# Kernel optimization log

Measured on AMD Instinct MI355X. Metric: run time of the kernel, lower is better.

## Reference

```python
import jax, jax.numpy as jnp
import numpy as np


def setup_inputs() -> dict:
    key = jax.random.key(0)
    k1, k2, k3, k4 = jax.random.split(key, 4)
    B, C, H, W = 8, 256, 64, 64
    x = jax.random.normal(k1, (B, C, H, W), dtype=jnp.float32)
    wq = jax.random.normal(k2, (1, C), dtype=jnp.float32) * (1.0 / np.sqrt(C))
    wk = jax.random.normal(k3, (1, C), dtype=jnp.float32) * (1.0 / np.sqrt(C))
    wv = jax.random.normal(k4, (C, C), dtype=jnp.float32) * (1.0 / np.sqrt(C))
    gamma = jnp.zeros((1,), dtype=jnp.float32)
    return {"x": x, "wq": wq, "wk": wk, "wv": wv, "gamma": gamma}


def reference(x, wq, wk, wv, gamma):
    B, C, H, W = x.shape
    N = H * W
    xf = x.reshape(B, C, N)                      # [B, C, N]
    # 1x1 convs == channel matmuls
    f = jnp.einsum('oc,bcn->bon', wq, xf)        # [B, 1, N]
    g = jnp.einsum('oc,bcn->bon', wk, xf)        # [B, 1, N]
    h = jnp.einsum('oc,bcn->bon', wv, xf)        # [B, C, N]
    # scores[b, i, j] = f[b, 0, i] * g[b, 0, j]  -> [B, N, N]
    scores = jnp.einsum('bi,bj->bij', f[:, 0, :], g[:, 0, :])
    # softmax over dim=1 (rows), matching torch F.softmax(..., dim=1)
    beta = jax.nn.softmax(scores, axis=1)        # [B, N, N]
    gam = gamma[0]
    o = (1.0 - gam) * jnp.einsum('bcn,bnm->bcm', h, beta) + gam * xf
    return o.reshape(B, C, H, W)
```

## Files before the change

### kernel.cpp

```cpp
#include <hip/hip_runtime.h>
#include <math.h>

#define BQ 8
#define CQ 256
#define NQ 4096
#define MT 128
#define NSUP 64

typedef short s16x8 __attribute__((ext_vector_type(8)));
typedef short s16x4 __attribute__((ext_vector_type(4)));
typedef float f32x4 __attribute__((ext_vector_type(4)));
typedef unsigned int uint;

static __device__ __forceinline__ float4 ld4(const float* p) { return *(const float4*)p; }

static constexpr float LOG2E = 1.4426950408889634f;

static __device__ __forceinline__ short f2bf(float f) {
    return __builtin_bit_cast(short, (__bf16)f);
}
static __device__ __forceinline__ uint fkey(float f) {
    uint b = __builtin_bit_cast(uint, f);
    return b ^ (0x80000000u | (uint)((int)b >> 31));
}
static __device__ __forceinline__ float fdec(uint u) {
    uint b = (u & 0x80000000u) ? (u ^ 0x80000000u) : ~u;
    return __builtin_bit_cast(float, b);
}

__global__ void k_fg(const float* __restrict__ x, const float* __restrict__ wq,
                     const float* __restrict__ wk, float* __restrict__ fs,
                     float* __restrict__ g, short* __restrict__ xbf,
                     uint* __restrict__ fmxu, uint* __restrict__ fmnu) {
    int b = blockIdx.y;
    int t = threadIdx.x;
    int nl = (t & 31) * 2;
    int cg = t >> 5;
    int n = blockIdx.x * 64 + nl;
    const float* xb = x + (size_t)b * CQ * NQ + n;
    uint* xo = (uint*)(xbf + (size_t)b * CQ * NQ + n);
    float f0 = 0.f, f1 = 0.f, g0 = 0.f, g1 = 0.f;
    int c0 = cg * 32;
#pragma unroll 8
    for (int c = c0; c < c0 + 32; ++c) {
        float2 v = *(const float2*)&xb[(size_t)c * NQ];
        f0 = fmaf(wq[c], v.x, f0);
        f1 = fmaf(wq[c], v.y, f1);
        g0 = fmaf(wk[c], v.x, g0);
        g1 = fmaf(wk[c], v.y, g1);
        uint p = (uint)(unsigned short)f2bf(v.x) | ((uint)(unsigned short)f2bf(v.y) << 16);
        xo[c * (NQ / 2)] = p;
    }
    __shared__ float sf[8][64], sg2[8][64];
    sf[cg][nl] = f0;  sf[cg][nl + 1] = f1;
    sg2[cg][nl] = g0; sg2[cg][nl + 1] = g1;
    __syncthreads();
    if (t < 64) {
        float f = 0.f, gg = 0.f;
#pragma unroll
        for (int i = 0; i < 8; ++i) { f += sf[i][t]; gg += sg2[i][t]; }
        f *= LOG2E;
        fs[b * NQ + blockIdx.x * 64 + t] = f;
        g[b * NQ + blockIdx.x * 64 + t]  = gg;
        float mx = f, mn = f;
#pragma unroll
        for (int off = 32; off; off >>= 1) {
            mx = fmaxf(mx, __shfl_xor(mx, off));
            mn = fminf(mn, __shfl_xor(mn, off));
        }
        if (t == 0) {
            atomicMax(&fmxu[b], fkey(mx));
            atomicMin(&fmnu[b], fkey(mn));
        }
    }
}

#define FLDS_OFF 131072
#define ZBUF_OFF 147456
#define SMEM_BYTES 149504

__global__ void __launch_bounds__(1024, 4) k_attn(
    const short* __restrict__ xbf, const float* __restrict__ fsp,
    const float* __restrict__ gp, const uint* __restrict__ fmxu,
    const uint* __restrict__ fmnu, const float* __restrict__ wv,
    const float* __restrict__ x, const float* __restrict__ gamma,
    float* __restrict__ out) {
    __shared__ __align__(16) char smem[SMEM_BYTES];

    int bid = blockIdx.x;
    int b = bid & 7;
    int mblk = bid >> 3;
    int m0 = mblk * MT;
    int tid = threadIdx.x;
    int l = tid & 63;
    int w = tid >> 6;
    int ws = w & 1;
    int wm = (w >> 1) & 3;
    int wc = w >> 3;
    int q = l >> 4;
    int cr = l & 15;
    int qp16 = (q ^ ((cr >> 1) & 3)) * 16;

    const short* xb = xbf + (size_t)b * CQ * NQ;
    const float* fb = fsp + b * NQ;

    int dst0 = tid * 16;
    int dst1 = tid * 16 + 16384;
    int srow = tid >> 2;
    int slq = (tid & 3) ^ ((srow >> 1) & 3);
    const short* src0 = xb + (size_t)srow * NQ + slq * 8;
    const short* src1 = src0 + 32;

    __builtin_amdgcn_global_load_lds(
        (const __attribute__((address_space(1))) void*)(fb + tid * 4),
        (__attribute__((address_space(3))) void*)(smem + FLDS_OFF + tid * 16), 16, 0, 0);
    __builtin_amdgcn_global_load_lds(
        (const __attribute__((address_space(1))) void*)src0,
        (__attribute__((address_space(3))) void*)(smem + dst0), 16, 0, 0);
    __builtin_amdgcn_global_load_lds(
        (const __attribute__((address_space(1))) void*)src1,
        (__attribute__((address_space(3))) void*)(smem + dst1), 16, 0, 0);
    src0 += 64;
    src1 += 64;

    float fmx = fdec(fmxu[b]), fmn = fdec(fmnu[b]);
    const float* gb = gp + b * NQ;
    float gj[2], nM[2], zac[2];
#pragma unroll
    for (int jm = 0; jm < 2; ++jm) {
        float gv = gb[m0 + wm * 32 + jm * 16 + cr];
        gj[jm] = gv;
        nM[jm] = -((gv >= 0.f) ? gv * fmx : gv * fmn);
        zac[jm] = 0.f;
    }

    f32x4 acc[8][2];
#pragma unroll
    for (int jc = 0; jc < 8; ++jc)
#pragma unroll
        for (int jm = 0; jm < 2; ++jm) acc[jc][jm] = (f32x4){0.f, 0.f, 0.f, 0.f};

    __syncthreads();

    for (int s = 0; s < NSUP; ++s) {
        if (s < NSUP - 1) {
            char* nbuf = smem + ((s + 1) & 1) * 32768;
            __builtin_amdgcn_global_load_lds(
                (const __attribute__((address_space(1))) void*)src0,
                (__attribute__((address_space(3))) void*)(nbuf + dst0), 16, 0, 0);
            __builtin_amdgcn_global_load_lds(
                (const __attribute__((address_space(1))) void*)src1,
                (__attribute__((address_space(3))) void*)(nbuf + dst1), 16, 0, 0);
            src0 += 64;
            src1 += 64;
        }
        int chunk = 2 * s + ws;
        const char* cbuf = smem + (s & 1) * 32768 + ws * 16384;
        const float* fls = (const float*)(smem + FLDS_OFF) + chunk * 32;
        float4 fqa = *(const float4*)(fls + q * 8);
        float4 fqb = *(const float4*)(fls + q * 8 + 4);
        float fq[8] = {fqa.x, fqa.y, fqa.z, fqa.w, fqb.x, fqb.y, fqb.z, fqb.w};
        s16x8 bv[2];
#pragma unroll
        for (int jm = 0; jm < 2; ++jm) {
            float z = zac[jm];
#pragma unroll
            for (int i = 0; i < 8; ++i) {
                float e = __builtin_amdgcn_exp2f(fmaf(fq[i], gj[jm], nM[jm]));
                z += e;
                bv[jm][i] = f2bf(e);
            }
            zac[jm] = z;
        }
#pragma unroll
        for (int jc = 0; jc < 8; ++jc) {
            s16x8 av = *(const s16x8*)(cbuf + (wc * 128 + jc * 16 + cr) * 64 + qp16);
            acc[jc][0] = __builtin_amdgcn_mfma_f32_16x16x32_bf16(av, bv[0], acc[jc][0], 0, 0, 0);
            acc[jc][1] = __builtin_amdgcn_mfma_f32_16x16x32_bf16(av, bv[1], acc[jc][1], 0, 0, 0);
        }
        __syncthreads();
    }

    float zf[2];
#pragma unroll
    for (int jm = 0; jm < 2; ++jm) {
        float z = zac[jm];
        z += __shfl_xor(z, 16);
        z += __shfl_xor(z, 32);
        zf[jm] = z;
    }
    float* zb = (float*)(smem + ZBUF_OFF);
    if (q == 0) {
#pragma unroll
        for (int jm = 0; jm < 2; ++jm) zb[w * 32 + jm * 16 + cr] = zf[jm];
    }
    __syncthreads();
#pragma unroll
    for (int jm = 0; jm < 2; ++jm) zf[jm] += zb[(w ^ 1) * 32 + jm * 16 + cr];

    {
        int p = wc * 4 + wm;
        float* mrg = (float*)(smem + p * 16384);
        if (ws == 1) {
#pragma unroll
            for (int jc = 0; jc < 8; ++jc)
#pragma unroll
                for (int jm = 0; jm < 2; ++jm)
                    *(f32x4*)(mrg + ((jc * 2 + jm) * 64 + l) * 4) = acc[jc][jm];
        }
        __syncthreads();
        if (ws == 0) {
#pragma unroll
            for (int jc = 0; jc < 8; ++jc)
#pragma unroll
                for (int jm = 0; jm < 2; ++jm) {
                    f32x4 o = *(const f32x4*)(mrg + ((jc * 2 + jm) * 64 + l) * 4);
                    acc[jc][jm] += o;
                }
        }
        __syncthreads();
    }

    if (ws == 0) {
        float rzl[2];
#pragma unroll
        for (int jm = 0; jm < 2; ++jm) rzl[jm] = 1.0f / zf[jm];
#pragma unroll
        for (int jc = 0; jc < 8; ++jc) {
#pragma unroll
            for (int jm = 0; jm < 2; ++jm) {
                int mloc = wm * 32 + jm * 16 + cr;
                int cb = (wc * 256 + jc * 32 + q * 8) ^ ((mloc & 7) << 4);
                s16x4 v;
#pragma unroll
                for (int r = 0; r < 4; ++r) v[r] = f2bf(acc[jc][jm][r] * rzl[jm]);
                *(s16x4*)(smem + mloc * 512 + cb) = v;
            }
        }
    }
    __syncthreads();

    int co0 = w * 16;
    f32x4 acc2[8];
#pragma unroll
    for (int jm2 = 0; jm2 < 8; ++jm2) acc2[jm2] = (f32x4){0.f, 0.f, 0.f, 0.f};

#pragma unroll 2
    for (int ks = 0; ks < 8; ++ks) {
        s16x8 a2;
        {
            const float* wr = wv + (size_t)(co0 + cr) * CQ + ks * 32 + q * 8;
            float4 wa = ld4(wr);
            float4 wb = ld4(wr + 4);
            a2[0] = f2bf(wa.x); a2[1] = f2bf(wa.y);
            a2[2] = f2bf(wa.z); a2[3] = f2bf(wa.w);
            a2[4] = f2bf(wb.x); a2[5] = f2bf(wb.y);
            a2[6] = f2bf(wb.z); a2[7] = f2bf(wb.w);
        }
#pragma unroll
        for (int jm2 = 0; jm2 < 8; ++jm2) {
            int mloc = jm2 * 16 + cr;
            s16x8 b2 = *(const s16x8*)(smem + mloc * 512 + ((ks * 64 + q * 16) ^ ((mloc & 7) << 4)));
            acc2[jm2] = __builtin_amdgcn_mfma_f32_16x16x32_bf16(a2, b2, acc2[jm2], 0, 0, 0);
        }
    }

    float gam = gamma[0];
    float omg = 1.f - gam;
    if (gam != 0.f) {
#pragma unroll
        for (int jm2 = 0; jm2 < 8; ++jm2)
#pragma unroll
            for (int r = 0; r < 4; ++r) {
                int c_out = co0 + q * 4 + r;
                size_t idx = ((size_t)b * CQ + c_out) * NQ + m0 + jm2 * 16 + cr;
                __builtin_nontemporal_store(
                    fmaf(gam, x[idx], acc2[jm2][r] * omg), out + idx);
            }
    } else {
#pragma unroll
        for (int jm2 = 0; jm2 < 8; ++jm2)
#pragma unroll
            for (int r = 0; r < 4; ++r) {
                int c_out = co0 + q * 4 + r;
                size_t idx = ((size_t)b * CQ + c_out) * NQ + m0 + jm2 * 16 + cr;
                __builtin_nontemporal_store(acc2[jm2][r] * omg, out + idx);
            }
    }
}

extern "C" void kernel_launch(void* const* d_in, const int* in_sizes, int n_in,
                              void* d_out, int out_size, void* d_ws, size_t ws_size,
                              hipStream_t stream) {
    const float* x     = (const float*)d_in[0];
    const float* wq    = (const float*)d_in[1];
    const float* wk    = (const float*)d_in[2];
    const float* wv    = (const float*)d_in[3];
    const float* gamma = (const float*)d_in[4];
    float* out = (float*)d_out;

    float* ws  = (float*)d_ws;
    float* fs  = ws;
    float* g   = ws + BQ * NQ;
    uint* fmxu = (uint*)(ws + 2 * BQ * NQ);
    uint* fmnu = fmxu + 8;
    short* xbf = (short*)(ws + 2 * BQ * NQ + 64);

    hipMemsetAsync(fmxu, 0x00, 32, stream);
    hipMemsetAsync(fmnu, 0xFF, 32, stream);
    hipLaunchKernelGGL(k_fg, dim3(NQ / 64, BQ), dim3(256), 0, stream,
                       x, wq, wk, fs, g, xbf, fmxu, fmnu);
    hipLaunchKernelGGL(k_attn, dim3(BQ * (NQ / MT)), dim3(1024), 0, stream,
                       xbf, fs, g, fmxu, fmnu, wv, x, gamma, out);
}
```

Baseline: 117.3 us.

## Triple-buffer x tiles with vmcnt waits and compute softmax denominators via MFMA

```diff
diff --git a/kernel.cpp b/kernel.cpp
--- a/kernel.cpp
+++ b/kernel.cpp
@@ -75,9 +75,9 @@
     }
 }
 
-#define FLDS_OFF 131072
-#define ZBUF_OFF 147456
-#define SMEM_BYTES 149504
+#define FLDS_OFF 98304
+#define ZBUF_OFF 131072
+#define SMEM_BYTES 133120
 
 __global__ void __launch_bounds__(1024, 4) k_attn(
     const short* __restrict__ xbf, const float* __restrict__ fsp,
@@ -104,103 +104,99 @@
     const short* xb = xbf + (size_t)b * CQ * NQ;
     const float* fb = fsp + b * NQ;
 
-    int dst0 = tid * 16;
-    int dst1 = tid * 16 + 16384;
     int srow = tid >> 2;
-    int slq = (tid & 3) ^ ((srow >> 1) & 3);
-    const short* src0 = xb + (size_t)srow * NQ + slq * 8;
-    const short* src1 = src0 + 32;
+    int sl = (tid & 3) ^ ((srow >> 1) & 3);
+    const short* srcb = xb + (size_t)srow * NQ + sl * 8;
+    int dst = tid * 16;
 
     __builtin_amdgcn_global_load_lds(
         (const __attribute__((address_space(1))) void*)(fb + tid * 4),
-        (__attribute__((address_space(3))) void*)(smem + FLDS_OFF + tid * 16), 16, 0, 0);
-    __builtin_amdgcn_global_load_lds(
-        (const __attribute__((address_space(1))) void*)src0,
-        (__attribute__((address_space(3))) void*)(smem + dst0), 16, 0, 0);
-    __builtin_amdgcn_global_load_lds(
-        (const __attribute__((address_space(1))) void*)src1,
-        (__attribute__((address_space(3))) void*)(smem + dst1), 16, 0, 0);
-    src0 += 64;
-    src1 += 64;
+        (__attribute__((address_space(3))) void*)(smem + FLDS_OFF + dst), 16, 0, 0);
+#pragma unroll
+    for (int k = 0; k < 4; ++k) {
+        __builtin_amdgcn_global_load_lds(
+            (const __attribute__((address_space(1))) void*)(srcb + k * 32),
+            (__attribute__((address_space(3))) void*)(smem + k * 16384 + dst), 16, 0, 0);
+    }
 
     float fmx = fdec(fmxu[b]), fmn = fdec(fmnu[b]);
     const float* gb = gp + b * NQ;
-    float gj[2], nM[2], zac[2];
+    float gj[2], nM[2];
 #pragma unroll
     for (int jm = 0; jm < 2; ++jm) {
         float gv = gb[m0 + wm * 32 + jm * 16 + cr];
         gj[jm] = gv;
         nM[jm] = -((gv >= 0.f) ? gv * fmx : gv * fmn);
-        zac[jm] = 0.f;
-    }
+    }
+    s16x8 ones;
+#pragma unroll
+    for (int i = 0; i < 8; ++i) ones[i] = (short)0x3F80;
 
     f32x4 acc[8][2];
 #pragma unroll
     for (int jc = 0; jc < 8; ++jc)
 #pragma unroll
         for (int jm = 0; jm < 2; ++jm) acc[jc][jm] = (f32x4){0.f, 0.f, 0.f, 0.f};
-
-    __syncthreads();
-
-    for (int s = 0; s < NSUP; ++s) {
-        if (s < NSUP - 1) {
-            char* nbuf = smem + ((s + 1) & 1) * 32768;
+    f32x4 accz[2] = {(f32x4){0.f, 0.f, 0.f, 0.f}, (f32x4){0.f, 0.f, 0.f, 0.f}};
+
+    asm volatile("s_waitcnt vmcnt(4)" ::: "memory");
+    __builtin_amdgcn_s_barrier();
+    const float* fl0 = (const float*)(smem + FLDS_OFF);
+    float4 fqa = *(const float4*)(fl0 + ws * 32 + q * 8);
+    float4 fqb = *(const float4*)(fl0 + ws * 32 + q * 8 + 4);
+
+    int rs = 0;
+    int ssl = 4;
+    for (int p = 0; p < NSUP; ++p) {
+        asm volatile("s_waitcnt vmcnt(2)" ::: "memory");
+        __builtin_amdgcn_s_barrier();
+        {
+            int chA = (2 * p + 4) & 127;
             __builtin_amdgcn_global_load_lds(
-                (const __attribute__((address_space(1))) void*)src0,
-                (__attribute__((address_space(3))) void*)(nbuf + dst0), 16, 0, 0);
+                (const __attribute__((address_space(1))) void*)(srcb + chA * 32),
+                (__attribute__((address_space(3))) void*)(smem + ssl * 16384 + dst), 16, 0, 0);
             __builtin_amdgcn_global_load_lds(
-                (const __attribute__((address_space(1))) void*)src1,
-                (__attribute__((address_space(3))) void*)(nbuf + dst1), 16, 0, 0);
-            src0 += 64;
-            src1 += 64;
-        }
-        int chunk = 2 * s + ws;
-        const char* cbuf = smem + (s & 1) * 32768 + ws * 16384;
-        const float* fls = (const float*)(smem + FLDS_OFF) + chunk * 32;
-        float4 fqa = *(const float4*)(fls + q * 8);
-        float4 fqb = *(const float4*)(fls + q * 8 + 4);
+                (const __attribute__((address_space(1))) void*)(srcb + (chA + 1) * 32),
+                (__attribute__((address_space(3))) void*)(smem + (ssl + 1) * 16384 + dst), 16, 0, 0);
+        }
         float fq[8] = {fqa.x, fqa.y, fqa.z, fqa.w, fqb.x, fqb.y, fqb.z, fqb.w};
         s16x8 bv[2];
 #pragma unroll
         for (int jm = 0; jm < 2; ++jm) {
-            float z = zac[jm];
-#pragma unroll
-            for (int i = 0; i < 8; ++i) {
-                float e = __builtin_amdgcn_exp2f(fmaf(fq[i], gj[jm], nM[jm]));
-                z += e;
-                bv[jm][i] = f2bf(e);
-            }
-            zac[jm] = z;
-        }
+#pragma unroll
+            for (int i = 0; i < 8; ++i)
+                bv[jm][i] = f2bf(__builtin_amdgcn_exp2f(fmaf(fq[i], gj[jm], nM[jm])));
+        }
+        accz[0] = __builtin_amdgcn_mfma_f32_16x16x32_bf16(ones, bv[0], accz[0], 0, 0, 0);
+        accz[1] = __builtin_amdgcn_mfma_f32_16x16x32_bf16(ones, bv[1], accz[1], 0, 0, 0);
+        {
+            int cn = (2 * p + 2 + ws) & 127;
+            fqa = *(const float4*)(fl0 + cn * 32 + q * 8);
+            fqb = *(const float4*)(fl0 + cn * 32 + q * 8 + 4);
+        }
+        const char* cbuf = smem + (rs + ws) * 16384;
+        __builtin_amdgcn_s_setprio(1);
 #pragma unroll
         for (int jc = 0; jc < 8; ++jc) {
             s16x8 av = *(const s16x8*)(cbuf + (wc * 128 + jc * 16 + cr) * 64 + qp16);
             acc[jc][0] = __builtin_amdgcn_mfma_f32_16x16x32_bf16(av, bv[0], acc[jc][0], 0, 0, 0);
             acc[jc][1] = __builtin_amdgcn_mfma_f32_16x16x32_bf16(av, bv[1], acc[jc][1], 0, 0, 0);
         }
-        __syncthreads();
-    }
-
-    float zf[2];
-#pragma unroll
-    for (int jm = 0; jm < 2; ++jm) {
-        float z = zac[jm];
-        z += __shfl_xor(z, 16);
-        z += __shfl_xor(z, 32);
-        zf[jm] = z;
-    }
-    float* zb = (float*)(smem + ZBUF_OFF);
-    if (q == 0) {
-#pragma unroll
-        for (int jm = 0; jm < 2; ++jm) zb[w * 32 + jm * 16 + cr] = zf[jm];
+        __builtin_amdgcn_s_setprio(0);
+        rs += 2;  if (rs >= 6) rs -= 6;
+        ssl += 2; if (ssl >= 6) ssl -= 6;
     }
     __syncthreads();
-#pragma unroll
-    for (int jm = 0; jm < 2; ++jm) zf[jm] += zb[(w ^ 1) * 32 + jm * 16 + cr];
-
+
+    float zf[2] = {accz[0][0], accz[1][0]};
     {
-        int p = wc * 4 + wm;
-        float* mrg = (float*)(smem + p * 16384);
+        float* zb = (float*)(smem + ZBUF_OFF);
+        if (q == 0) {
+#pragma unroll
+            for (int jm = 0; jm < 2; ++jm) zb[w * 32 + jm * 16 + cr] = zf[jm];
+        }
+        int p8 = wc * 4 + wm;
+        float* mrg = (float*)(smem + p8 * 16384);
         if (ws == 1) {
 #pragma unroll
             for (int jc = 0; jc < 8; ++jc)
@@ -218,6 +214,8 @@
                     acc[jc][jm] += o;
                 }
         }
+#pragma unroll
+        for (int jm = 0; jm < 2; ++jm) zf[jm] += zb[(w ^ 1) * 32 + jm * 16 + cr];
         __syncthreads();
     }
 
```

New measurement: 123.5 us. 1.05x slower.
